# Performance work log

Measured on AMD Instinct MI355X. Metric: run time of the kernel, lower is better.

Reference implementation:

```python
import jax, jax.numpy as jnp
import numpy as np

B, N, D, OUT = 4, 4096, 2048, 2048
E, RANK, TOP_K = 8, 16, 2
ALPHA = 16.0
SCALING = ALPHA / RANK


def setup_inputs() -> dict:
    key = jax.random.key(0)
    k1, k2, k3, k4 = jax.random.split(key, 4)
    x = jax.random.normal(k1, (B, N, D), dtype=jnp.float32)
    weight = jax.random.normal(k2, (OUT, D), dtype=jnp.float32) * (1.0 / np.sqrt(D))
    router_w = jax.random.normal(k3, (E, D), dtype=jnp.float32) * 0.02
    experts_A = jax.random.normal(k4, (E, D, RANK), dtype=jnp.float32) * (1.0 / np.sqrt(RANK))
    # experts_B is zero-initialized in the module; use small random values so the
    # LoRA branch contributes non-trivially to the output for kernel testing.
    experts_B = jax.random.normal(jax.random.fold_in(key, 5), (E, RANK, OUT), dtype=jnp.float32) * 0.02
    return {"x": x, "weight": weight, "router_w": router_w,
            "experts_A": experts_A, "experts_B": experts_B}


def reference(x, weight, router_w, experts_A, experts_B):
    # base = F.linear(x, weight)  (no bias)
    base = jnp.einsum('bnd,od->bno', x, weight)
    # router logits: x @ W_r^T -> (B, N, E)
    logits = jnp.einsum('bnd,ed->bne', x, router_w)
    # top-k sparse routing: keep top-k logits, set rest to -inf, softmax
    topk_vals, topk_idx = jax.lax.top_k(logits, TOP_K)  # (B,N,K)
    keep = jax.nn.one_hot(topk_idx, E, dtype=jnp.bool_).any(axis=-2)  # (B,N,E)
    masked = jnp.where(keep, logits, -jnp.inf)
    router_weights = jax.nn.softmax(masked, axis=-1)  # (B,N,E)
    # per-expert low-rank down/up projection, weighted by router
    lora_down = jnp.einsum('bnd,edr->bner', x, experts_A)  # (B,N,E,rank)
    weighted = lora_down * router_weights[..., None]
    moe_out = jnp.einsum('bner,erd->bnd', weighted, experts_B)  # (B,N,OUT)
    return base + SCALING * moe_out
```

## Files before the change

kernel.cpp:

```cpp
#include <hip/hip_runtime.h>
#include <stdint.h>

#define D_DIM 2048
#define OUT_DIM 2048
#define NTOK 16384
#define SCALING 1.0f
#define NT32 68

typedef unsigned short u16;
typedef __attribute__((ext_vector_type(8))) short s16x8;
typedef __attribute__((ext_vector_type(4))) float f32x4;

#define WZ_OFF  0u
#define AZ_OFF  8388608u
#define BZ_OFF  8912896u
#define CZ_OFF  9437184u
#define XB_OFF  14155776u
#define WS_BIG   81264640u

__device__ inline u16 f2bf(float f) {
  union { float f; uint32_t u; } v; v.f = f;
  uint32_t u = v.u;
  u += 0x7FFFu + ((u >> 16) & 1u);
  return (u16)(u >> 16);
}

__device__ inline int swz32(int c, int row) {
  return (c & ~31) | (((((c >> 3) & 3) ^ ((row >> 1) & 3))) << 3) | (c & 7);
}

#define GLDS(gp, lp) __builtin_amdgcn_global_load_lds( \
    (const __attribute__((address_space(1))) void*)(gp), \
    (__attribute__((address_space(3))) void*)(lp), 16, 0, 0)

__global__ __launch_bounds__(256) void k_prep(const float* __restrict__ W,
                                              const float* __restrict__ A,
                                              const float* __restrict__ Bf,
                                              u16* __restrict__ Wz,
                                              u16* __restrict__ Az,
                                              u16* __restrict__ Bz) {
  int bid = blockIdx.x;
  if (bid < 4096) {
    int idx = bid * 256 + threadIdx.x;
    int o  = idx >> 9;
    int k0 = (idx & 511) * 4;
    const float4 v = *(const float4*)&W[(size_t)o * D_DIM + k0];
    int dst = swz32(k0, o);
    uint32_t p0 = (uint32_t)f2bf(v.x) | ((uint32_t)f2bf(v.y) << 16);
    uint32_t p1 = (uint32_t)f2bf(v.z) | ((uint32_t)f2bf(v.w) << 16);
    *(uint2*)&Wz[(size_t)o * D_DIM + dst] = make_uint2(p0, p1);
    return;
  }
  if (bid < 5120) {
    int idx = (bid - 4096) * 256 + threadIdx.x;
    float v = A[idx];
    int r = idx & 15;
    int d = (idx >> 4) & 2047;
    int e = idx >> 15;
    int er = e * 16 + r;
    Az[(size_t)er * D_DIM + swz32(d, er)] = f2bf(v);
    return;
  }
  {
    int idx = (bid - 5120) * 256 + threadIdx.x;
    float v = Bf[idx];
    int er = idx >> 11;
    int o  = idx & 2047;
    Bz[(size_t)o * 128 + swz32(er, o)] = f2bf(v);
  }
}

__global__ __launch_bounds__(256) void k_router_lora(
    const float* __restrict__ x, const float* __restrict__ rw,
    const u16* __restrict__ Az, u16* __restrict__ xb, u16* __restrict__ Cz) {
  __shared__ u16 Axl[2][64 * 64];
  __shared__ u16 Bzl[2][128 * 64];
  __shared__ float w8s[64 * 8];
  int tid = threadIdx.x, lane = tid & 63, wid = tid >> 6;
  int t0 = blockIdx.x * 64;
  const int l15 = lane & 15;

  f32x4 acc[8];
#pragma unroll
  for (int n = 0; n < 8; ++n) acc[n] = (f32x4){0.f, 0.f, 0.f, 0.f};
  float lgp[4][8];
#pragma unroll
  for (int i = 0; i < 4; ++i)
#pragma unroll
    for (int e = 0; e < 8; ++e) lgp[i][e] = 0.f;

  auto stage = [&](int kc, int buf) {
    bool real = (kc <= 31);
    if (!real) kc = 31;
    const int c4 = (tid & 15) * 4;
    float4 rv[8];
    if (real) {
#pragma unroll
      for (int e = 0; e < 8; ++e)
        rv[e] = *(const float4*)&rw[(size_t)e * D_DIM + kc * 64 + c4];
    }
#pragma unroll
    for (int i = 0; i < 4; ++i) {
      int row = i * 16 + (tid >> 4);
      float4 v = *(const float4*)&x[(size_t)(t0 + row) * D_DIM + kc * 64 + c4];
      uint32_t p0 = (uint32_t)f2bf(v.x) | ((uint32_t)f2bf(v.y) << 16);
      uint32_t p1 = (uint32_t)f2bf(v.z) | ((uint32_t)f2bf(v.w) << 16);
      *(uint2*)&xb[(size_t)(t0 + row) * D_DIM + swz32(kc * 64 + c4, row)] =
          make_uint2(p0, p1);
      *(uint2*)&Axl[buf][row * 64 + swz32(c4, row)] = make_uint2(p0, p1);
      if (real) {
#pragma unroll
        for (int e = 0; e < 8; ++e) {
          lgp[i][e] = fmaf(v.x, rv[e].x, lgp[i][e]);
          lgp[i][e] = fmaf(v.y, rv[e].y, lgp[i][e]);
          lgp[i][e] = fmaf(v.z, rv[e].z, lgp[i][e]);
          lgp[i][e] = fmaf(v.w, rv[e].w, lgp[i][e]);
        }
      }
    }
#pragma unroll
    for (int i = 0; i < 4; ++i) {
      const u16* g = Az + (size_t)(i * 32 + (tid >> 3)) * D_DIM + kc * 64 + (tid & 7) * 8;
      GLDS(g, &Bzl[buf][0] + i * 2048 + tid * 8);
    }
  };

  stage(0, 0);
  asm volatile("s_waitcnt vmcnt(0) lgkmcnt(0)" ::: "memory");
  __builtin_amdgcn_s_barrier();

  for (int kc = 0; kc < 32; ++kc) {
    int cur = kc & 1;
    stage(kc + 1, cur ^ 1);
    const int g = (lane >> 4) ^ ((l15 >> 1) & 3);
#pragma unroll
    for (int kk = 0; kk < 2; ++kk) {
      s16x8 af = *(const s16x8*)&Axl[cur][(wid * 16 + l15) * 64 + kk * 32 + g * 8];
#pragma unroll
      for (int nf = 0; nf < 8; ++nf) {
        s16x8 bf = *(const s16x8*)&Bzl[cur][(nf * 16 + l15) * 64 + kk * 32 + g * 8];
        acc[nf] = __builtin_amdgcn_mfma_f32_16x16x32_bf16(af, bf, acc[nf], 0, 0, 0);
      }
    }
    asm volatile("s_waitcnt vmcnt(0) lgkmcnt(0)" ::: "memory");
    __builtin_amdgcn_s_barrier();
  }

#pragma unroll
  for (int i = 0; i < 4; ++i) {
#pragma unroll
    for (int e = 0; e < 8; ++e) {
      float v = lgp[i][e];
      v += __shfl_xor(v, 1, 64);
      v += __shfl_xor(v, 2, 64);
      v += __shfl_xor(v, 4, 64);
      v += __shfl_xor(v, 8, 64);
      lgp[i][e] = v;
    }
    float l0 = lgp[i][0]; int i0 = 0;
#pragma unroll
    for (int e = 1; e < 8; ++e) if (lgp[i][e] > l0) { l0 = lgp[i][e]; i0 = e; }
    float l1 = -3e38f; int i1 = 0;
#pragma unroll
    for (int e = 0; e < 8; ++e) if (e != i0 && lgp[i][e] > l1) { l1 = lgp[i][e]; i1 = e; }
    float e1 = expf(l1 - l0);
    float inv = 1.f / (1.f + e1);
    if (l15 < 8) {
      int row = i * 16 + (tid >> 4);
      w8s[row * 8 + l15] =
          (l15 == i0) ? inv * SCALING : (l15 == i1) ? e1 * inv * SCALING : 0.f;
    }
  }
  __syncthreads();

#pragma unroll
  for (int q = 0; q < 4; ++q) {
    int rl = wid * 16 + (lane >> 4) * 4 + q;
#pragma unroll
    for (int nf = 0; nf < 8; ++nf) {
      float v = acc[nf][q] * w8s[rl * 8 + nf];
      int er = nf * 16 + l15;
      Cz[(size_t)(t0 + rl) * 128 + swz32(er, rl)] = f2bf(v);
    }
  }
}

__global__ __launch_bounds__(256, 3) void k_main128(const u16* __restrict__ xb,
                                                    const u16* __restrict__ Wz,
                                                    const u16* __restrict__ Cz,
                                                    const u16* __restrict__ Bz,
                                                    float* __restrict__ out) {
  __shared__ u16 AL[2][4096];
  __shared__ u16 BL[2][4096];
  const int tid = threadIdx.x, lane = tid & 63;
  const int wid = tid >> 6, wm = wid >> 1, wn = wid & 1;
  int bid = blockIdx.x;
  int swz = (bid & 7) * 256 + (bid >> 3);
  int mt = swz >> 4, nt = swz & 15;
  int t0 = mt * 128, o0 = nt * 128;
  const int l15 = lane & 15;
  const int gA = (lane >> 4) ^ ((l15 >> 1) & 3);
  const int aoff = (wm * 64 + l15) * 32 + gA * 8;
  const int boff = (wn * 64 + l15) * 32 + gA * 8;
  const int srow = tid >> 2, sc8 = (tid & 3) * 8;

  f32x4 acc[4][4];
#pragma unroll
  for (int m = 0; m < 4; ++m)
#pragma unroll
    for (int n = 0; n < 4; ++n) acc[m][n] = (f32x4){0.f, 0.f, 0.f, 0.f};
  s16x8 aA[4], bA[4], aB[4], bB[4];

  auto stg = [&](int t, int bufi) {
    if (t > NT32 - 1) t = NT32 - 1;
    const u16 *sa, *sb; int lda, ldb, ca;
    if (t < 64) { sa = xb; lda = D_DIM; sb = Wz; ldb = D_DIM; ca = t * 32; }
    else        { sa = Cz; lda = 128;   sb = Bz; ldb = 128;   ca = (t - 64) * 32; }
#pragma unroll
    for (int i = 0; i < 2; ++i) {
      const u16* g = sa + (size_t)(t0 + i * 64 + srow) * lda + ca + sc8;
      GLDS(g, &AL[bufi][0] + i * 2048 + tid * 8);
      const u16* h = sb + (size_t)(o0 + i * 64 + srow) * ldb + ca + sc8;
      GLDS(h, &BL[bufi][0] + i * 2048 + tid * 8);
    }
  };

#define RD(av, bv, bufi) do {                                            \
    _Pragma("unroll") for (int i_ = 0; i_ < 4; ++i_)                     \
      av[i_] = *(const s16x8*)&AL[bufi][aoff + i_ * 512];                \
    _Pragma("unroll") for (int j_ = 0; j_ < 4; ++j_)                     \
      bv[j_] = *(const s16x8*)&BL[bufi][boff + j_ * 512];                \
  } while (0)

#define MM(av, bv) do {                                                  \
    _Pragma("unroll") for (int mf_ = 0; mf_ < 4; ++mf_)                  \
      _Pragma("unroll") for (int nf_ = 0; nf_ < 4; ++nf_)                \
        acc[mf_][nf_] = __builtin_amdgcn_mfma_f32_16x16x32_bf16(         \
            av[mf_], bv[nf_], acc[mf_][nf_], 0, 0, 0);                   \
  } while (0)

  stg(0, 0);
  asm volatile("s_waitcnt vmcnt(0)" ::: "memory");
  __builtin_amdgcn_s_barrier();
  RD(aA, bA, 0);
  stg(1, 1);
  asm volatile("s_waitcnt vmcnt(0) lgkmcnt(0)" ::: "memory");
  __builtin_amdgcn_s_barrier();

  for (int jj = 0; jj < NT32; jj += 2) {
    RD(aB, bB, 1);
    stg(jj + 2, 0);
    MM(aA, bA);
    asm volatile("s_waitcnt vmcnt(0) lgkmcnt(0)" ::: "memory");
    __builtin_amdgcn_s_barrier();
    RD(aA, bA, 0);
    stg(jj + 3, 1);
    MM(aB, bB);
    asm volatile("s_waitcnt vmcnt(0) lgkmcnt(0)" ::: "memory");
    __builtin_amdgcn_s_barrier();
  }
#undef RD
#undef MM

#pragma unroll
  for (int mf = 0; mf < 4; ++mf)
#pragma unroll
    for (int q = 0; q < 4; ++q) {
      int row = t0 + wm * 64 + mf * 16 + (lane >> 4) * 4 + q;
#pragma unroll
      for (int nf = 0; nf < 4; ++nf) {
        int col = o0 + wn * 64 + nf * 16 + l15;
        out[(size_t)row * OUT_DIM + col] = acc[mf][nf][q];
      }
    }
}

extern "C" void kernel_launch(void* const* d_in, const int* in_sizes, int n_in,
                              void* d_out, int out_size, void* d_ws, size_t ws_size,
                              hipStream_t stream) {
  const float* x  = (const float*)d_in[0];
  const float* W  = (const float*)d_in[1];
  const float* rw = (const float*)d_in[2];
  const float* eA = (const float*)d_in[3];
  const float* eB = (const float*)d_in[4];
  float* out = (float*)d_out;
  char* ws = (char*)d_ws;
  if (ws_size < WS_BIG) return;

  u16* Wz = (u16*)(ws + WZ_OFF);
  u16* Az = (u16*)(ws + AZ_OFF);
  u16* Bz = (u16*)(ws + BZ_OFF);
  u16* Cz = (u16*)(ws + CZ_OFF);
  u16* xb = (u16*)(ws + XB_OFF);

  k_prep<<<6144, 256, 0, stream>>>(W, eA, eB, Wz, Az, Bz);
  k_router_lora<<<256, 256, 0, stream>>>(x, rw, Az, xb, Cz);
  k_main128<<<2048, 256, 0, stream>>>(xb, Wz, Cz, Bz, out);
}
```

Measured before the change: 257.8 us.

## Enlarge main GEMM tile to 256x256 with 4-stage LDS pipeline

The main fused GEMM moves from 128x128 tiles with 256 threads to 256x256 tiles with 512 threads. Each wave now computes a 128x64 sub-tile. Larger tiles cut global and L2 traffic per FLOP and raise MFMA work per LDS read. The double buffer becomes a 4-deep ring with partial vmcnt waits, so loads run further ahead of compute, and s_setprio raises priority around the MFMA bursts. In exchange, LDS use of 128KB likely allows only one block per CU, and the larger accumulator set raises register pressure.

```diff
diff --git a/kernel.cpp b/kernel.cpp
--- a/kernel.cpp
+++ b/kernel.cpp
@@ -185,31 +185,31 @@
   }
 }
 
-__global__ __launch_bounds__(256, 3) void k_main128(const u16* __restrict__ xb,
-                                                    const u16* __restrict__ Wz,
-                                                    const u16* __restrict__ Cz,
-                                                    const u16* __restrict__ Bz,
-                                                    float* __restrict__ out) {
-  __shared__ u16 AL[2][4096];
-  __shared__ u16 BL[2][4096];
+__global__ __launch_bounds__(512, 2) void k_main32(const u16* __restrict__ xb,
+                                                   const u16* __restrict__ Wz,
+                                                   const u16* __restrict__ Cz,
+                                                   const u16* __restrict__ Bz,
+                                                   float* __restrict__ out) {
+  __shared__ u16 AL[4][8192];
+  __shared__ u16 BL[4][8192];
   const int tid = threadIdx.x, lane = tid & 63;
-  const int wid = tid >> 6, wm = wid >> 1, wn = wid & 1;
+  const int wid = tid >> 6, wm = wid >> 2, wn = wid & 3;
   int bid = blockIdx.x;
-  int swz = (bid & 7) * 256 + (bid >> 3);
-  int mt = swz >> 4, nt = swz & 15;
-  int t0 = mt * 128, o0 = nt * 128;
+  int swz = (bid & 7) * 64 + (bid >> 3);
+  int mt = swz >> 3, nt = swz & 7;
+  int t0 = mt * 256, o0 = nt * 256;
   const int l15 = lane & 15;
   const int gA = (lane >> 4) ^ ((l15 >> 1) & 3);
-  const int aoff = (wm * 64 + l15) * 32 + gA * 8;
+  const int aoff = (wm * 128 + l15) * 32 + gA * 8;
   const int boff = (wn * 64 + l15) * 32 + gA * 8;
   const int srow = tid >> 2, sc8 = (tid & 3) * 8;
 
-  f32x4 acc[4][4];
-#pragma unroll
-  for (int m = 0; m < 4; ++m)
+  f32x4 acc[8][4];
+#pragma unroll
+  for (int m = 0; m < 8; ++m)
 #pragma unroll
     for (int n = 0; n < 4; ++n) acc[m][n] = (f32x4){0.f, 0.f, 0.f, 0.f};
-  s16x8 aA[4], bA[4], aB[4], bB[4];
+  s16x8 aA[8], bA[4], aB[8], bB[4];
 
   auto stg = [&](int t, int bufi) {
     if (t > NT32 - 1) t = NT32 - 1;
@@ -218,55 +218,60 @@
     else        { sa = Cz; lda = 128;   sb = Bz; ldb = 128;   ca = (t - 64) * 32; }
 #pragma unroll
     for (int i = 0; i < 2; ++i) {
-      const u16* g = sa + (size_t)(t0 + i * 64 + srow) * lda + ca + sc8;
-      GLDS(g, &AL[bufi][0] + i * 2048 + tid * 8);
-      const u16* h = sb + (size_t)(o0 + i * 64 + srow) * ldb + ca + sc8;
-      GLDS(h, &BL[bufi][0] + i * 2048 + tid * 8);
+      const u16* g = sa + (size_t)(t0 + i * 128 + srow) * lda + ca + sc8;
+      GLDS(g, &AL[bufi][0] + i * 4096 + tid * 8);
+    }
+#pragma unroll
+    for (int i = 0; i < 2; ++i) {
+      const u16* g = sb + (size_t)(o0 + i * 128 + srow) * ldb + ca + sc8;
+      GLDS(g, &BL[bufi][0] + i * 4096 + tid * 8);
     }
   };
 
-#define RD(av, bv, bufi) do {                                            \
-    _Pragma("unroll") for (int i_ = 0; i_ < 4; ++i_)                     \
-      av[i_] = *(const s16x8*)&AL[bufi][aoff + i_ * 512];                \
-    _Pragma("unroll") for (int j_ = 0; j_ < 4; ++j_)                     \
-      bv[j_] = *(const s16x8*)&BL[bufi][boff + j_ * 512];                \
+#define RD(av, bv, bufi) do {                                           \
+    const u16* ap_ = &AL[bufi][aoff];                                   \
+    const u16* bp_ = &BL[bufi][boff];                                   \
+    _Pragma("unroll") for (int i_ = 0; i_ < 8; ++i_)                    \
+      av[i_] = *(const s16x8*)(ap_ + i_ * 512);                         \
+    _Pragma("unroll") for (int j_ = 0; j_ < 4; ++j_)                    \
+      bv[j_] = *(const s16x8*)(bp_ + j_ * 512);                         \
   } while (0)
 
-#define MM(av, bv) do {                                                  \
-    _Pragma("unroll") for (int mf_ = 0; mf_ < 4; ++mf_)                  \
-      _Pragma("unroll") for (int nf_ = 0; nf_ < 4; ++nf_)                \
-        acc[mf_][nf_] = __builtin_amdgcn_mfma_f32_16x16x32_bf16(         \
-            av[mf_], bv[nf_], acc[mf_][nf_], 0, 0, 0);                   \
+#define MM(av, bv) do {                                                 \
+    __builtin_amdgcn_s_setprio(1);                                      \
+    _Pragma("unroll") for (int mf_ = 0; mf_ < 8; ++mf_)                 \
+      _Pragma("unroll") for (int nf_ = 0; nf_ < 4; ++nf_)               \
+        acc[mf_][nf_] = __builtin_amdgcn_mfma_f32_16x16x32_bf16(        \
+            av[mf_], bv[nf_], acc[mf_][nf_], 0, 0, 0);                  \
+    __builtin_amdgcn_s_setprio(0);                                      \
   } while (0)
 
-  stg(0, 0);
-  asm volatile("s_waitcnt vmcnt(0)" ::: "memory");
+  stg(0, 0); stg(1, 1); stg(2, 2);
+  asm volatile("s_waitcnt vmcnt(4)" ::: "memory");
   __builtin_amdgcn_s_barrier();
   RD(aA, bA, 0);
-  stg(1, 1);
+
+  for (int jj = 0; jj < NT32; jj += 2) {
+    RD(aB, bB, (jj + 1) & 3);
+    MM(aA, bA);
+    stg(jj + 3, (jj + 3) & 3);
+    asm volatile("s_waitcnt vmcnt(4)" ::: "memory");
+    __builtin_amdgcn_s_barrier();
+    RD(aA, bA, (jj + 2) & 3);
+    MM(aB, bB);
+    stg(jj + 4, (jj + 4) & 3);
+    asm volatile("s_waitcnt vmcnt(4)" ::: "memory");
+    __builtin_amdgcn_s_barrier();
+  }
   asm volatile("s_waitcnt vmcnt(0) lgkmcnt(0)" ::: "memory");
-  __builtin_amdgcn_s_barrier();
-
-  for (int jj = 0; jj < NT32; jj += 2) {
-    RD(aB, bB, 1);
-    stg(jj + 2, 0);
-    MM(aA, bA);
-    asm volatile("s_waitcnt vmcnt(0) lgkmcnt(0)" ::: "memory");
-    __builtin_amdgcn_s_barrier();
-    RD(aA, bA, 0);
-    stg(jj + 3, 1);
-    MM(aB, bB);
-    asm volatile("s_waitcnt vmcnt(0) lgkmcnt(0)" ::: "memory");
-    __builtin_amdgcn_s_barrier();
-  }
 #undef RD
 #undef MM
 
 #pragma unroll
-  for (int mf = 0; mf < 4; ++mf)
+  for (int mf = 0; mf < 8; ++mf)
 #pragma unroll
     for (int q = 0; q < 4; ++q) {
-      int row = t0 + wm * 64 + mf * 16 + (lane >> 4) * 4 + q;
+      int row = t0 + wm * 128 + mf * 16 + (lane >> 4) * 4 + q;
 #pragma unroll
       for (int nf = 0; nf < 4; ++nf) {
         int col = o0 + wn * 64 + nf * 16 + l15;
@@ -295,5 +300,5 @@
 
   k_prep<<<6144, 256, 0, stream>>>(W, eA, eB, Wz, Az, Bz);
   k_router_lora<<<256, 256, 0, stream>>>(x, rw, Az, xb, Cz);
-  k_main128<<<2048, 256, 0, stream>>>(xb, Wz, Cz, Bz, out);
-}
+  k_main32<<<512, 512, 0, stream>>>(xb, Wz, Cz, Bz, out);
+}
```

Result: faster. 225.5 us (-12.5%).
